# Kernel optimization log

Hardware: AMD Instinct MI355X
Metric: run time of the kernel (lower is better)

The kernel has to match this reference:

```python
import jax, jax.numpy as jnp
import numpy as np

NEG_INF = -jnp.inf

def _sage_conv(x_src, x_dst, src, dst, Wl, bl, Wr, aggr, num_nodes):
    # messages = source features gathered along edges  [E, d]
    msgs = x_src[src]
    if aggr == 'mean':
        s = jax.ops.segment_sum(msgs, dst, num_segments=num_nodes)
        cnt = jax.ops.segment_sum(jnp.ones((src.shape[0],), x_src.dtype), dst, num_segments=num_nodes)
        agg = s / jnp.maximum(cnt, 1.0)[:, None]
    else:  # max; isolated targets -> 0 (PyG scatter-max fill)
        m = jax.ops.segment_max(msgs, dst, num_segments=num_nodes)
        agg = jnp.where(jnp.isfinite(m), m, 0.0)
    return agg @ Wl.T + bl + x_dst @ Wr.T

def setup_inputs() -> dict:
    key = jax.random.key(0)
    ks = jax.random.split(key, 12)
    N, E, D, H, C, L = 40000, 640000, 128, 128, 64, 2
    sc = 0.05
    return {
        'x': jax.random.normal(ks[0], (N, D), jnp.float32),
        'edge_index0': jax.random.randint(ks[1], (2, E), 0, N, jnp.int64),
        'edge_index1': jax.random.randint(ks[2], (2, E), 0, N, jnp.int64),
        'Wl_mean': jax.random.normal(ks[3], (L, H, D), jnp.float32) * sc,
        'bl_mean': jax.random.normal(ks[4], (L, H), jnp.float32) * sc,
        'Wr_mean': jax.random.normal(ks[5], (L, H, D), jnp.float32) * sc,
        'Wl_max': jax.random.normal(ks[6], (L, H, D), jnp.float32) * sc,
        'bl_max': jax.random.normal(ks[7], (L, H), jnp.float32) * sc,
        'Wr_max': jax.random.normal(ks[8], (L, H, D), jnp.float32) * sc,
        'post_W': jax.random.normal(ks[9], (C, 2 * L * H), jnp.float32) * sc,
        'post_b': jax.random.normal(ks[10], (C,), jnp.float32) * sc,
    }

def reference(x, edge_index0, edge_index1, Wl_mean, bl_mean, Wr_mean, Wl_max, bl_max, Wr_max, post_W, post_b):
    N = x.shape[0]
    edge_sets = [edge_index0, edge_index1]
    L = len(edge_sets)
    h = x
    all_layers = []
    for i, ei in enumerate(edge_sets):
        src, dst = ei[0], ei[1]
        x_mean = _sage_conv(h, h, src, dst, Wl_mean[i], bl_mean[i], Wr_mean[i], 'mean', N)
        x_max = _sage_conv(h, h, src, dst, Wl_max[i], bl_max[i], Wr_max[i], 'max', N)
        all_layers.append(x_mean)
        all_layers.append(x_max)
        if i != L - 1:
            h = jax.nn.relu(h)  # note: original never replaces x with conv output
    x_final = jnp.concatenate(all_layers, axis=1) @ post_W.T + post_b
    return jax.nn.log_softmax(x_final, axis=-1)
```

## Files before the change

kernel.cpp:

```cpp
#include <hip/hip_runtime.h>
#include <cstdint>
#include <cstddef>

constexpr int FD = 128;
constexpr int CC = 64;
constexpr int KTOT = 768;
constexpr int CAP = 48;
constexpr int SS = 4096;
constexpr int CSTR = 16;

typedef __attribute__((ext_vector_type(8))) short short8;
typedef __attribute__((ext_vector_type(4))) float f32x4;

__device__ __forceinline__ float u2f(unsigned u) {
  union { unsigned u; float f; } v; v.u = u; return v.f;
}
__device__ __forceinline__ unsigned f2bf(float f) {
  union { float f; unsigned u; } v; v.f = f;
  return (v.u + 0x7FFFu + ((v.u >> 16) & 1u)) >> 16;
}
__device__ __forceinline__ unsigned pack2(float a, float b) {
  return f2bf(a) | (f2bf(b) << 16);
}
__device__ __forceinline__ unsigned relu_pk(unsigned v) {
  unsigned m = ((v >> 15) & 0x10001u) * 0xFFFFu;
  return v & ~m;
}

__global__ __launch_bounds__(256) void zero_kernel(uint4* __restrict__ p, int n4) {
  int i = blockIdx.x * 256 + threadIdx.x;
  if (i < n4) p[i] = make_uint4(0u, 0u, 0u, 0u);
}

__global__ __launch_bounds__(256) void prebuild_kernel(
    const float* __restrict__ x, uint4* __restrict__ xbf4, uint4* __restrict__ xrbf4,
    int n8,
    const int* __restrict__ e0, int E0,
    const int* __restrict__ e1, int E1,
    int* __restrict__ cnt, unsigned short* __restrict__ csrf, int N, int NC, int nbuild,
    const float* __restrict__ Wl_mean, const float* __restrict__ bl_mean,
    const float* __restrict__ Wr_mean, const float* __restrict__ Wl_max,
    const float* __restrict__ bl_max,  const float* __restrict__ Wr_max,
    const float* __restrict__ postW,   const float* __restrict__ postb,
    unsigned short* __restrict__ Mbf, float* __restrict__ cb)
{
  if (blockIdx.x < nbuild) {
    const int b = blockIdx.x;
    const int c = b & 7;
    const int t = b >> 3;
    const int nst0 = (E0 + SS - 1) / SS;
    const int* e; int E; int s; int stripe;
    if (t < nst0) { e = e0; E = E0; s = 0; stripe = t; }
    else          { e = e1; E = E1; s = 1; stripe = t - nst0; }
    const int lo = c * NC;
    const int hi = min(N, lo + NC);
    const int i0 = stripe * SS;
    const int i1 = min(E, i0 + SS);
    int* mycnt = cnt + (size_t)(s * 8 + c) * NC * CSTR;
    unsigned short* mycsr = csrf + (size_t)(s * 8 + c) * NC * CAP;
    const bool vec4 = ((E & 3) == 0);

    for (int i = i0 + threadIdx.x * 4; i < i1; i += 1024) {
      if (vec4 && i + 3 < i1) {
        int4 d4 = *(const int4*)(e + E + i);
        int dd[4] = {d4.x, d4.y, d4.z, d4.w};
        #pragma unroll
        for (int u = 0; u < 4; ++u) {
          if (dd[u] >= lo && dd[u] < hi) {
            int srcv = e[i + u];
            int n_ = dd[u] - lo;
            int pos = atomicAdd(&mycnt[n_ * CSTR], 1);
            if (pos < CAP) mycsr[(size_t)pos * NC + n_] = (unsigned short)srcv;
          }
        }
      } else {
        for (int u = 0; u < 4 && i + u < i1; ++u) {
          int dd = e[E + i + u];
          if (dd >= lo && dd < hi) {
            int srcv = e[i + u];
            int n_ = dd - lo;
            int pos = atomicAdd(&mycnt[n_ * CSTR], 1);
            if (pos < CAP) mycsr[(size_t)pos * NC + n_] = (unsigned short)srcv;
          }
        }
      }
    }
  } else {
    const int gtid = (blockIdx.x - nbuild) * 256 + threadIdx.x;
    const int gsz = (gridDim.x - nbuild) * 256;

    for (int t = gtid; t < n8; t += gsz) {
      float4 a = *(const float4*)(x + (size_t)t * 8);
      float4 b = *(const float4*)(x + (size_t)t * 8 + 4);
      uint4 q;
      q.x = pack2(a.x, a.y); q.y = pack2(a.z, a.w);
      q.z = pack2(b.x, b.y); q.w = pack2(b.z, b.w);
      xbf4[t] = q;
      uint4 r;
      r.x = relu_pk(q.x); r.y = relu_pk(q.y);
      r.z = relu_pk(q.z); r.w = relu_pk(q.w);
      xrbf4[t] = r;
    }

    for (int t = gtid; t < KTOT * CC; t += gsz) {
      int c  = t & (CC - 1);
      int k  = t >> 6;
      int blk = k >> 7;
      int kk  = k & 127;
      const float* pw = postW + (size_t)c * 512;
      float acc = 0.f;
      if (blk < 4) {
        const float* W;
        if (blk == 0)      W = Wl_mean;
        else if (blk == 1) W = Wl_max;
        else if (blk == 2) W = Wl_mean + 128 * 128;
        else               W = Wl_max + 128 * 128;
        const float* pp = pw + blk * 128;
        #pragma unroll 8
        for (int h = 0; h < 128; ++h) acc += pp[h] * W[h * 128 + kk];
      } else if (blk == 4) {
        #pragma unroll 8
        for (int h = 0; h < 128; ++h)
          acc += pw[h] * Wr_mean[h * 128 + kk] + pw[128 + h] * Wr_max[h * 128 + kk];
      } else {
        const float* Wm = Wr_mean + 128 * 128;
        const float* Wx = Wr_max + 128 * 128;
        #pragma unroll 8
        for (int h = 0; h < 128; ++h)
          acc += pw[256 + h] * Wm[h * 128 + kk] + pw[384 + h] * Wx[h * 128 + kk];
      }
      Mbf[(size_t)c * KTOT + k] = (unsigned short)f2bf(acc);

      if (t < CC) {
        const float* pwc = postW + (size_t)t * 512;
        float b = postb[t];
        for (int h = 0; h < 128; ++h) {
          b += bl_mean[h]        * pwc[h]
             + bl_max[h]         * pwc[128 + h]
             + bl_mean[128 + h]  * pwc[256 + h]
             + bl_max[128 + h]   * pwc[384 + h];
        }
        cb[t] = b;
      }
    }
  }
}

__global__ __launch_bounds__(256) void agg_kernel(
    const unsigned* __restrict__ xbf, const unsigned* __restrict__ xrbf,
    const int* __restrict__ cnt, const unsigned short* __restrict__ csrf,
    unsigned* __restrict__ aggbf, int N, int NC)
{
  int gw = (blockIdx.x * 256 + threadIdx.x) >> 6;
  int lane = threadIdx.x & 63;
  if (gw >= 2 * N) return;
  const int layer = (gw >= N) ? 1 : 0;
  const int node = gw - layer * N;
  const int cls = node / NC;
  const int n_ = node - cls * NC;
  const int reg = layer * 8 + cls;
  const int deg = min(cnt[((size_t)reg * NC + n_) * CSTR], CAP);
  const char* csb = (const char*)(csrf + (size_t)reg * NC * CAP);
  const char* xl  = (const char*)(layer ? xrbf : xbf);
  const int half = lane >> 5;
  const int hl = lane & 31;
  const unsigned lb = (unsigned)hl * 8u;

  const int n0 = (deg + 1) >> 1;
  const int cbeg = half ? n0 : 0;
  const int ce   = half ? deg : n0;
  const int cnth = ce - cbeg;
  const unsigned strideB = (unsigned)NC * 2u;

  float s0 = 0.f, s1 = 0.f, s2 = 0.f, s3 = 0.f;
  float m0 = -INFINITY, m1 = -INFINITY, m2 = -INFINITY, m3 = -INFINITY;

  if (cnth > 0) {
    unsigned off = (unsigned)cbeg * strideB + (unsigned)n_ * 2u;
    const unsigned omax = (unsigned)(ce - 1) * strideB + (unsigned)n_ * 2u;
    const int niter = (cnth + 7) >> 3;
    for (int it = 0; it < niter; ++it) {
      unsigned o[8];
      #pragma unroll
      for (int u = 0; u < 8; ++u) o[u] = min(off + (unsigned)u * strideB, omax);
      off += 8u * strideB;
      unsigned idx[8];
      #pragma unroll
      for (int u = 0; u < 8; ++u) idx[u] = *(const unsigned short*)(csb + o[u]);
      uint2 g[8];
      #pragma unroll
      for (int u = 0; u < 8; ++u)
        g[u] = *(const uint2*)(xl + ((idx[u] << 8) + lb));
      #pragma unroll
      for (int u = 0; u < 8; ++u) {
        float a0 = u2f(g[u].x << 16);
        float a1 = u2f(g[u].x & 0xffff0000u);
        float a2 = u2f(g[u].y << 16);
        float a3 = u2f(g[u].y & 0xffff0000u);
        s0 += a0; s1 += a1; s2 += a2; s3 += a3;
        m0 = fmaxf(m0, a0); m1 = fmaxf(m1, a1);
        m2 = fmaxf(m2, a2); m3 = fmaxf(m3, a3);
      }
    }
    const int npad = niter * 8 - cnth;
    if (npad > 0) {
      unsigned idx = *(const unsigned short*)(csb + omax);
      uint2 g = *(const uint2*)(xl + ((idx << 8) + lb));
      float fn = (float)npad;
      s0 = fmaf(-fn, u2f(g.x << 16), s0);
      s1 = fmaf(-fn, u2f(g.x & 0xffff0000u), s1);
      s2 = fmaf(-fn, u2f(g.y << 16), s2);
      s3 = fmaf(-fn, u2f(g.y & 0xffff0000u), s3);
    }
  }

  s0 += __shfl_xor(s0, 32); s1 += __shfl_xor(s1, 32);
  s2 += __shfl_xor(s2, 32); s3 += __shfl_xor(s3, 32);
  m0 = fmaxf(m0, __shfl_xor(m0, 32)); m1 = fmaxf(m1, __shfl_xor(m1, 32));
  m2 = fmaxf(m2, __shfl_xor(m2, 32)); m3 = fmaxf(m3, __shfl_xor(m3, 32));

  if (half == 0) {
    float inv = 1.f / (float)(deg > 0 ? deg : 1);
    if (deg == 0) { m0 = 0.f; m1 = 0.f; m2 = 0.f; m3 = 0.f; }
    unsigned* am = aggbf + (size_t)(layer * 2)     * N * 64;
    unsigned* ax = aggbf + (size_t)(layer * 2 + 1) * N * 64;
    size_t o = (size_t)node * 64 + hl * 2;
    *(uint2*)(am + o) = make_uint2(pack2(s0 * inv, s1 * inv), pack2(s2 * inv, s3 * inv));
    *(uint2*)(ax + o) = make_uint2(pack2(m0, m1), pack2(m2, m3));
  }
}

__global__ __launch_bounds__(256) void gemm_kernel(
    const unsigned* __restrict__ aggbf, const unsigned* __restrict__ xbf,
    const unsigned* __restrict__ xrbf,
    const unsigned short* __restrict__ Mbf, const float* __restrict__ cb,
    float* __restrict__ out, int N)
{
  const int tid = threadIdx.x;
  const int w = tid >> 6, l = tid & 63;
  const int l15 = l & 15, lg = l >> 4;
  const int kg = lg * 8;
  const size_t N64 = (size_t)N * 64;
  const int rowb = blockIdx.x * 64 + w * 16;
  const int r0 = rowb + l15;
  const size_t a0r = (size_t)min(r0, N - 1) * 64;

  f32x4 acc[4];
  #pragma unroll
  for (int j = 0; j < 4; ++j) acc[j] = (f32x4){0.f, 0.f, 0.f, 0.f};

  #pragma unroll
  for (int b6 = 0; b6 < 6; ++b6) {
    const unsigned* Ap = (b6 < 4) ? (aggbf + (size_t)b6 * N64)
                                  : (b6 == 4 ? xbf : xrbf);
    #pragma unroll
    for (int ss = 0; ss < 4; ++ss) {
      const int k0 = b6 * 128 + ss * 32;
      const int ko = (ss * 32 + kg) >> 1;
      uint4 ua = *(const uint4*)(Ap + a0r + ko);
      short8 af = __builtin_bit_cast(short8, ua);
      #pragma unroll
      for (int fc = 0; fc < 4; ++fc) {
        const int c = fc * 16 + l15;
        uint4 qb = *(const uint4*)(Mbf + (size_t)c * KTOT + k0 + kg);
        short8 bf = __builtin_bit_cast(short8, qb);
        acc[fc] = __builtin_amdgcn_mfma_f32_16x16x32_bf16(af, bf, acc[fc], 0, 0, 0);
      }
    }
  }

  float bias[4];
  #pragma unroll
  for (int fc = 0; fc < 4; ++fc) bias[fc] = cb[fc * 16 + l15];

  #pragma unroll
  for (int i = 0; i < 4; ++i) {
    int row = rowb + lg * 4 + i;
    float z0 = acc[0][i] + bias[0];
    float z1 = acc[1][i] + bias[1];
    float z2 = acc[2][i] + bias[2];
    float z3 = acc[3][i] + bias[3];
    float m = fmaxf(fmaxf(z0, z1), fmaxf(z2, z3));
    #pragma unroll
    for (int o = 1; o < 16; o <<= 1) m = fmaxf(m, __shfl_xor(m, o));
    float s = expf(z0 - m) + expf(z1 - m) + expf(z2 - m) + expf(z3 - m);
    #pragma unroll
    for (int o = 1; o < 16; o <<= 1) s += __shfl_xor(s, o);
    float lse = m + logf(s);
    if (row < N) {
      size_t ob = (size_t)row * CC + l15;
      out[ob]      = z0 - lse;
      out[ob + 16] = z1 - lse;
      out[ob + 32] = z2 - lse;
      out[ob + 48] = z3 - lse;
    }
  }
}

extern "C" void kernel_launch(void* const* d_in, const int* in_sizes, int n_in,
                              void* d_out, int out_size, void* d_ws, size_t ws_size,
                              hipStream_t stream)
{
  const float* x       = (const float*)d_in[0];
  const int*   e0      = (const int*)d_in[1];
  const int*   e1      = (const int*)d_in[2];
  const float* Wl_mean = (const float*)d_in[3];
  const float* bl_mean = (const float*)d_in[4];
  const float* Wr_mean = (const float*)d_in[5];
  const float* Wl_max  = (const float*)d_in[6];
  const float* bl_max  = (const float*)d_in[7];
  const float* Wr_max  = (const float*)d_in[8];
  const float* postW   = (const float*)d_in[9];
  const float* postb   = (const float*)d_in[10];
  float* out = (float*)d_out;

  const int N  = in_sizes[0] / FD;
  const int E0 = in_sizes[1] / 2;
  const int E1 = in_sizes[2] / 2;
  const int NC = (N + 7) / 8;

  char* ws = (char*)d_ws;
  size_t off = 0;
  auto alloc = [&](size_t bytes) -> void* {
    void* p = ws + off;
    off = (off + bytes + 255) & ~(size_t)255;
    return p;
  };
  unsigned short* Mbf  = (unsigned short*)alloc((size_t)KTOT * CC * 2);
  float*          cbv  = (float*)alloc(CC * 4);
  int*            cnt  = (int*)alloc((size_t)16 * NC * CSTR * 4);
  unsigned short* csrf = (unsigned short*)alloc((size_t)16 * NC * CAP * 2);
  unsigned*       xbf  = (unsigned*)alloc((size_t)N * 64 * 4);
  unsigned*       xrbf = (unsigned*)alloc((size_t)N * 64 * 4);
  unsigned*       aggbf= (unsigned*)alloc((size_t)4 * N * 64 * 4);
  (void)ws_size; (void)n_in; (void)out_size;

  const int cnt4 = 16 * NC * CSTR / 4;
  zero_kernel<<<dim3((cnt4 + 255) / 256), dim3(256), 0, stream>>>((uint4*)cnt, cnt4);

  const int nst = (E0 + SS - 1) / SS + (E1 + SS - 1) / SS;
  const int nbuild = 8 * nst;
  const int n8 = N * 16;
  prebuild_kernel<<<dim3(nbuild + 1024), dim3(256), 0, stream>>>(
      x, (uint4*)xbf, (uint4*)xrbf, n8,
      e0, E0, e1, E1, cnt, csrf, N, NC, nbuild,
      Wl_mean, bl_mean, Wr_mean, Wl_max, bl_max, Wr_max, postW, postb, Mbf, cbv);

  const int aggBlocks = (2 * N * 64 + 255) / 256;
  agg_kernel<<<dim3(aggBlocks), dim3(256), 0, stream>>>(
      xbf, xrbf, cnt, csrf, aggbf, N, NC);

  gemm_kernel<<<dim3((N + 63) / 64), dim3(256), 0, stream>>>(
      aggbf, xbf, xrbf, Mbf, cbv, out, N);
}
```

Before: 256.4 us.

## Store CSR neighbor lists node-major and load indices as vectors

Switches the per-region CSR neighbor array from slot-major (pos*NC+n) to node-major (n*CAP+pos), so each node's neighbor indices are contiguous. The aggregation kernel then reads 8 indices with a single 16-byte load instead of 8 strided 2-byte loads, and the two half-waves interleave 8-neighbor groups rather than splitting the list in halves. Partial groups replace the old negative-padding correction with clamped indices and masked sums. The build step's scattered writes become node-contiguous, which may change write coalescing.

```diff
diff --git a/kernel.cpp b/kernel.cpp
--- a/kernel.cpp
+++ b/kernel.cpp
@@ -70,7 +70,7 @@
             int srcv = e[i + u];
             int n_ = dd[u] - lo;
             int pos = atomicAdd(&mycnt[n_ * CSTR], 1);
-            if (pos < CAP) mycsr[(size_t)pos * NC + n_] = (unsigned short)srcv;
+            if (pos < CAP) mycsr[(size_t)n_ * CAP + pos] = (unsigned short)srcv;
           }
         }
       } else {
@@ -80,7 +80,7 @@
             int srcv = e[i + u];
             int n_ = dd - lo;
             int pos = atomicAdd(&mycnt[n_ * CSTR], 1);
-            if (pos < CAP) mycsr[(size_t)pos * NC + n_] = (unsigned short)srcv;
+            if (pos < CAP) mycsr[(size_t)n_ * CAP + pos] = (unsigned short)srcv;
           }
         }
       }
@@ -160,57 +160,62 @@
   const int n_ = node - cls * NC;
   const int reg = layer * 8 + cls;
   const int deg = min(cnt[((size_t)reg * NC + n_) * CSTR], CAP);
-  const char* csb = (const char*)(csrf + (size_t)reg * NC * CAP);
-  const char* xl  = (const char*)(layer ? xrbf : xbf);
+  const unsigned short* csn = csrf + (size_t)reg * NC * CAP + (size_t)n_ * CAP;
+  const char* xl = (const char*)(layer ? xrbf : xbf);
   const int half = lane >> 5;
   const int hl = lane & 31;
   const unsigned lb = (unsigned)hl * 8u;
 
-  const int n0 = (deg + 1) >> 1;
-  const int cbeg = half ? n0 : 0;
-  const int ce   = half ? deg : n0;
-  const int cnth = ce - cbeg;
-  const unsigned strideB = (unsigned)NC * 2u;
-
   float s0 = 0.f, s1 = 0.f, s2 = 0.f, s3 = 0.f;
   float m0 = -INFINITY, m1 = -INFINITY, m2 = -INFINITY, m3 = -INFINITY;
 
-  if (cnth > 0) {
-    unsigned off = (unsigned)cbeg * strideB + (unsigned)n_ * 2u;
-    const unsigned omax = (unsigned)(ce - 1) * strideB + (unsigned)n_ * 2u;
-    const int niter = (cnth + 7) >> 3;
-    for (int it = 0; it < niter; ++it) {
-      unsigned o[8];
-      #pragma unroll
-      for (int u = 0; u < 8; ++u) o[u] = min(off + (unsigned)u * strideB, omax);
-      off += 8u * strideB;
-      unsigned idx[8];
-      #pragma unroll
-      for (int u = 0; u < 8; ++u) idx[u] = *(const unsigned short*)(csb + o[u]);
-      uint2 g[8];
+  const int ngroups = (deg + 7) >> 3;
+  for (int g = half; g < ngroups; g += 2) {
+    const int base = g * 8;
+    const int rem = deg - base;
+    unsigned idx[8];
+    if (rem >= 8) {
+      uint4 iv = *(const uint4*)(csn + base);
+      idx[0] = iv.x & 0xffffu; idx[1] = iv.x >> 16;
+      idx[2] = iv.y & 0xffffu; idx[3] = iv.y >> 16;
+      idx[4] = iv.z & 0xffffu; idx[5] = iv.z >> 16;
+      idx[6] = iv.w & 0xffffu; idx[7] = iv.w >> 16;
+      uint2 gg[8];
       #pragma unroll
       for (int u = 0; u < 8; ++u)
-        g[u] = *(const uint2*)(xl + ((idx[u] << 8) + lb));
+        gg[u] = *(const uint2*)(xl + ((idx[u] << 8) + lb));
       #pragma unroll
       for (int u = 0; u < 8; ++u) {
-        float a0 = u2f(g[u].x << 16);
-        float a1 = u2f(g[u].x & 0xffff0000u);
-        float a2 = u2f(g[u].y << 16);
-        float a3 = u2f(g[u].y & 0xffff0000u);
+        float a0 = u2f(gg[u].x << 16);
+        float a1 = u2f(gg[u].x & 0xffff0000u);
+        float a2 = u2f(gg[u].y << 16);
+        float a3 = u2f(gg[u].y & 0xffff0000u);
         s0 += a0; s1 += a1; s2 += a2; s3 += a3;
         m0 = fmaxf(m0, a0); m1 = fmaxf(m1, a1);
         m2 = fmaxf(m2, a2); m3 = fmaxf(m3, a3);
       }
-    }
-    const int npad = niter * 8 - cnth;
-    if (npad > 0) {
-      unsigned idx = *(const unsigned short*)(csb + omax);
-      uint2 g = *(const uint2*)(xl + ((idx << 8) + lb));
-      float fn = (float)npad;
-      s0 = fmaf(-fn, u2f(g.x << 16), s0);
-      s1 = fmaf(-fn, u2f(g.x & 0xffff0000u), s1);
-      s2 = fmaf(-fn, u2f(g.y << 16), s2);
-      s3 = fmaf(-fn, u2f(g.y & 0xffff0000u), s3);
+    } else {
+      #pragma unroll
+      for (int u = 0; u < 8; ++u) {
+        bool val = u < rem;
+        idx[u] = csn[base + (val ? u : rem - 1)];
+      }
+      uint2 gg[8];
+      #pragma unroll
+      for (int u = 0; u < 8; ++u)
+        gg[u] = *(const uint2*)(xl + ((idx[u] << 8) + lb));
+      #pragma unroll
+      for (int u = 0; u < 8; ++u) {
+        bool val = u < rem;
+        float a0 = u2f(gg[u].x << 16);
+        float a1 = u2f(gg[u].x & 0xffff0000u);
+        float a2 = u2f(gg[u].y << 16);
+        float a3 = u2f(gg[u].y & 0xffff0000u);
+        s0 += val ? a0 : 0.f;  s1 += val ? a1 : 0.f;
+        s2 += val ? a2 : 0.f;  s3 += val ? a3 : 0.f;
+        m0 = fmaxf(m0, a0); m1 = fmaxf(m1, a1);
+        m2 = fmaxf(m2, a2); m3 = fmaxf(m3, a3);
+      }
     }
   }
 
```

Result: no change. 252.7 us (-1.4%).
